# Optimization experiments

Hardware: AMD Instinct MI355X
Metric: run time of the kernel (lower is better)

## Reference

```python
import jax, jax.numpy as jnp
import numpy as np

N = 262144
C_IN = 128
C_OUT = 128
K = 9


def setup_inputs() -> dict:
    key = jax.random.key(0)
    k1, k2, k3, k4 = jax.random.split(key, 4)
    features = jax.random.normal(k1, (N, C_IN), dtype=jnp.float32)
    neigh_idx = jax.random.randint(k2, (N, K), 0, N, dtype=jnp.int64)
    # nn.Linear(9*in_channels, out_channels): weight [out, 9*in], bias [out]
    fan_in = K * C_IN
    W = jax.random.normal(k3, (C_OUT, fan_in), dtype=jnp.float32) / np.sqrt(fan_in)
    b = jax.random.normal(k4, (C_OUT,), dtype=jnp.float32) * 0.01
    return {"features": features, "neigh_idx": neigh_idx, "W": W, "b": b}


def reference(features, neigh_idx, W, b):
    n = features.shape[0]
    # pad row of zeros at index n; redirect -1 neighbors to it
    feat_padded = jnp.concatenate([features, jnp.zeros((1, features.shape[1]), features.dtype)], axis=0)
    gather_idx = jnp.where(neigh_idx == -1, n, neigh_idx)
    col = feat_padded[gather_idx]              # [N, 9, C_in]
    col_flat = col.reshape(n, -1)              # [N, 9*C_in]
    return col_flat @ W.T + b                  # [N, C_out]
```

## Files before the change

kernel.cpp:

```cpp
#include <hip/hip_runtime.h>


#define NPTS    262144
#define CIN     128
#define COUT    128
#define KNBR    9
#define KDIM    1152
#define NKS     72
#define NFRAGS  288
#define NFRAGS_PAD 296
#define MT      256

typedef __bf16  bf16x8 __attribute__((ext_vector_type(8)));
typedef float   f32x4  __attribute__((ext_vector_type(4)));
typedef float   f32x16 __attribute__((ext_vector_type(16)));

#define VMCNT(n) (((n) & 0xF) | (((n) >> 4) << 14) | (0xF << 8) | (7 << 4))

__global__ __launch_bounds__(256) void convert_feat_kernel(const float* __restrict__ f,
                                                           __bf16* __restrict__ fb) {
    size_t i = ((size_t)blockIdx.x * 256 + threadIdx.x) * 8;
    f32x4 a = __builtin_nontemporal_load((const f32x4*)(f + i));
    f32x4 b = __builtin_nontemporal_load((const f32x4*)(f + i + 4));
    bf16x8 o;
#pragma unroll
    for (int k = 0; k < 4; ++k) { o[k] = (__bf16)a[k]; o[k + 4] = (__bf16)b[k]; }
    *(bf16x8*)(fb + i) = o;
}

__global__ __launch_bounds__(256) void pack_w_kernel(const float* __restrict__ W,
                                                     __bf16* __restrict__ Wp,
                                                     __bf16* __restrict__ zrow_b) {
    if (blockIdx.x == NFRAGS / 4) {
        int t = threadIdx.x;
        if (t < CIN) zrow_b[t] = (__bf16)0.f;
        return;
    }
    int t    = blockIdx.x * 256 + threadIdx.x;
    int lane = t & 63;
    int frag = t >> 6;
    int nt = frag & 3;
    int ks = frag >> 2;
    int n  = nt * 32 + (lane & 31);
    int k0 = ks * 16 + (lane >> 5) * 8;
    const f32x4* src = (const f32x4*)(W + (size_t)n * KDIM + k0);
    f32x4 v0 = src[0], v1 = src[1];
    bf16x8 o;
#pragma unroll
    for (int i = 0; i < 4; ++i) { o[i] = (__bf16)v0[i]; o[i + 4] = (__bf16)v1[i]; }
    *(bf16x8*)(Wp + (size_t)frag * 512 + lane * 8) = o;
}

__global__ __launch_bounds__(256, 2) void qconv_kernel(
    const __bf16* __restrict__ featb,
    const int*    __restrict__ nidx,
    const __bf16* __restrict__ Wp,
    const __bf16* __restrict__ zrow,
    const float*  __restrict__ bias,
    float*        __restrict__ out)
{
    __shared__ __align__(16) char lds_raw[4 * 2 * 2 * 4096];

    const int tid  = threadIdx.x;
    const int lane = tid & 63;
    const int wave = tid >> 6;
    const int l31  = lane & 31;
    const int half = lane >> 5;
    const int rb   = blockIdx.x * MT;
    char* myLds = lds_raw + wave * 16384;

    const int srow = lane >> 3;
    const int schk = lane & 7;

    const int* ia[8];
#pragma unroll
    for (int n = 0; n < 8; ++n) {
        int rg = rb + (n >> 2) * 128 + wave * 32 + (n & 3) * 8 + srow;
        ia[n] = nidx + (size_t)rg * KNBR;
    }

    f32x16 acc[8];
#pragma unroll
    for (int a = 0; a < 8; ++a)
#pragma unroll
        for (int i = 0; i < 16; ++i) acc[a][i] = 0.f;

    const __bf16* Pst[8];
    int NPidx[8];
    bf16x8 Bb[3][4];

    auto convertP = [&](void) {
#pragma unroll
        for (int n = 0; n < 8; ++n)
            Pst[n] = (NPidx[n] >= 0) ? featb + (size_t)NPidx[n] * CIN : zrow;
    };
    auto stage_chunk = [&](int c) {
        const int buf  = c & 1;
        const int eoff = (c & 1) * 64 + (schk ^ srow) * 8;
#pragma unroll
        for (int n = 0; n < 8; ++n) {
            const int T = n >> 2, i = n & 3;
            const __bf16* g = Pst[n] + eoff;
            char* dst = myLds + buf * 8192 + T * 4096 + i * 1024;
            __builtin_amdgcn_global_load_lds(
                (const __attribute__((address_space(1))) void*)g,
                (__attribute__((address_space(3))) void*)dst,
                16, 0, 0);
        }
    };
    auto issueB = [&](int t) {
#pragma unroll
        for (int nt = 0; nt < 4; ++nt)
            Bb[t % 3][nt] = *(const bf16x8*)(Wp + (size_t)(t * 4 + nt) * 512 + lane * 8);
    };
    auto readA = [&](int buf, int T, int ksl) -> bf16x8 {
        const int s = (ksl * 2 + half) ^ (l31 & 7);
        return *(const bf16x8*)(myLds + buf * 8192 + T * 4096 + l31 * 128 + s * 16);
    };

#pragma unroll
    for (int n = 0; n < 8; ++n) NPidx[n] = ia[n][0];
    convertP();
    __builtin_amdgcn_sched_barrier(0);
    stage_chunk(0);
    __builtin_amdgcn_sched_barrier(0);
    issueB(0); issueB(1);

#pragma unroll
    for (int j = 0; j < KNBR; ++j) {
        __builtin_amdgcn_sched_barrier(0);
        if (j == 0) __builtin_amdgcn_s_waitcnt(VMCNT(8));
        else        __builtin_amdgcn_s_waitcnt(VMCNT(16));
        __builtin_amdgcn_sched_barrier(0);
        stage_chunk(2 * j + 1);
        __builtin_amdgcn_sched_barrier(0);
        {
            const int jn = (j + 1 < KNBR) ? j + 1 : KNBR - 1;
#pragma unroll
            for (int n = 0; n < 8; ++n) NPidx[n] = ia[n][jn];
#pragma unroll
            for (int ksl = 0; ksl < 4; ++ksl) {
                const int t = j * 8 + ksl;
                issueB(t + 2);
                bf16x8 a0 = readA(0, 0, ksl);
                bf16x8 a1 = readA(0, 1, ksl);
#pragma unroll
                for (int nt = 0; nt < 4; ++nt) {
                    acc[nt]     = __builtin_amdgcn_mfma_f32_32x32x16_bf16(a0, Bb[t % 3][nt], acc[nt], 0, 0, 0);
                    acc[4 + nt] = __builtin_amdgcn_mfma_f32_32x32x16_bf16(a1, Bb[t % 3][nt], acc[4 + nt], 0, 0, 0);
                }
            }
        }
        __builtin_amdgcn_sched_barrier(0);
        __builtin_amdgcn_s_waitcnt(VMCNT(24));
        __builtin_amdgcn_sched_barrier(0);
        convertP();
        stage_chunk(2 * j + 2);
        __builtin_amdgcn_sched_barrier(0);
#pragma unroll
        for (int ksl = 4; ksl < 8; ++ksl) {
            const int t = j * 8 + ksl;
            issueB(t + 2);
            bf16x8 a0 = readA(1, 0, ksl - 4);
            bf16x8 a1 = readA(1, 1, ksl - 4);
#pragma unroll
            for (int nt = 0; nt < 4; ++nt) {
                acc[nt]     = __builtin_amdgcn_mfma_f32_32x32x16_bf16(a0, Bb[t % 3][nt], acc[nt], 0, 0, 0);
                acc[4 + nt] = __builtin_amdgcn_mfma_f32_32x32x16_bf16(a1, Bb[t % 3][nt], acc[4 + nt], 0, 0, 0);
            }
        }
    }

#pragma unroll
    for (int nt = 0; nt < 4; ++nt) {
        const int col = nt * 32 + l31;
        const float bv = bias[col];
#pragma unroll
        for (int r = 0; r < 16; ++r) {
            const int row = (r & 3) + 8 * (r >> 2) + 4 * half;
            __builtin_nontemporal_store(acc[nt][r] + bv,
                &out[(size_t)(rb + wave * 32 + row) * COUT + col]);
            __builtin_nontemporal_store(acc[4 + nt][r] + bv,
                &out[(size_t)(rb + 128 + wave * 32 + row) * COUT + col]);
        }
    }
}

__global__ void qconv_naive(const float* __restrict__ feat, const int* __restrict__ nidx,
                            const float* __restrict__ W, const float* __restrict__ bias,
                            float* __restrict__ out) {
    int p = blockIdx.x, c = threadIdx.x;
    float s = bias[c];
    for (int j = 0; j < KNBR; ++j) {
        int g = nidx[(size_t)p * KNBR + j];
        if (g < 0) continue;
        const float* fr = feat + (size_t)g * CIN;
        const float* wr = W + (size_t)c * KDIM + j * CIN;
        for (int k = 0; k < CIN; ++k) s += fr[k] * wr[k];
    }
    out[(size_t)p * COUT + c] = s;
}

extern "C" void kernel_launch(void* const* d_in, const int* in_sizes, int n_in,
                              void* d_out, int out_size, void* d_ws, size_t ws_size,
                              hipStream_t stream) {
    const float* feat = (const float*)d_in[0];
    const int*   nidx = (const int*)d_in[1];
    const float* W    = (const float*)d_in[2];
    const float* bias = (const float*)d_in[3];
    float*       out  = (float*)d_out;

    const size_t FEATB_BYTES = (size_t)NPTS * CIN * 2;
    const size_t WP_BYTES    = (size_t)NFRAGS_PAD * 512 * 2;

    if (ws_size >= FEATB_BYTES + WP_BYTES + 512) {
        __bf16* featb  = (__bf16*)d_ws;
        __bf16* Wp     = (__bf16*)((char*)d_ws + FEATB_BYTES);
        __bf16* zrow_b = (__bf16*)((char*)d_ws + FEATB_BYTES + WP_BYTES);
        convert_feat_kernel<<<NPTS * CIN / (256 * 8), 256, 0, stream>>>(feat, featb);
        pack_w_kernel<<<NFRAGS / 4 + 1, 256, 0, stream>>>(W, Wp, zrow_b);
        qconv_kernel<<<NPTS / MT, 256, 0, stream>>>(featb, nidx, Wp, zrow_b, bias, out);
    } else {
        qconv_naive<<<NPTS, COUT, 0, stream>>>(feat, nidx, W, bias, out);
    }
}
```

Baseline: 358.8 us.

## Deepen gather pipeline by staging chunks earlier and use 32-bit gather offsets

Restructures the per-neighbor loop so each half-chunk's gather into LDS is issued one phase earlier, mid-way through the previous MFMA block after an LDS-read wait. This keeps two chunks in flight and hides gather latency better. Gather addresses become 32-bit byte offsets from the bf16 feature base, and the zero row is reached through a fixed offset instead of a separate pointer. The index-pointer arrays are collapsed into two base pointers. The risks are more VGPR pressure and the correctness of the hand-tuned vmcnt and lgkmcnt values, since an LDS buffer is overwritten while it may still be read.

```diff
diff --git a/kernel.cpp b/kernel.cpp
--- a/kernel.cpp
+++ b/kernel.cpp
@@ -6,16 +6,17 @@
 #define COUT    128
 #define KNBR    9
 #define KDIM    1152
-#define NKS     72
 #define NFRAGS  288
 #define NFRAGS_PAD 296
 #define MT      256
+#define ZOFFB   67411968u
 
 typedef __bf16  bf16x8 __attribute__((ext_vector_type(8)));
 typedef float   f32x4  __attribute__((ext_vector_type(4)));
 typedef float   f32x16 __attribute__((ext_vector_type(16)));
 
 #define VMCNT(n) (((n) & 0xF) | (((n) >> 4) << 14) | (0xF << 8) | (7 << 4))
+#define LGKM0    (0xF | (3 << 14) | (7 << 4))
 
 __global__ __launch_bounds__(256) void convert_feat_kernel(const float* __restrict__ f,
                                                            __bf16* __restrict__ fb) {
@@ -55,7 +56,6 @@
     const __bf16* __restrict__ featb,
     const int*    __restrict__ nidx,
     const __bf16* __restrict__ Wp,
-    const __bf16* __restrict__ zrow,
     const float*  __restrict__ bias,
     float*        __restrict__ out)
 {
@@ -71,13 +71,10 @@
 
     const int srow = lane >> 3;
     const int schk = lane & 7;
-
-    const int* ia[8];
-#pragma unroll
-    for (int n = 0; n < 8; ++n) {
-        int rg = rb + (n >> 2) * 128 + wave * 32 + (n & 3) * 8 + srow;
-        ia[n] = nidx + (size_t)rg * KNBR;
-    }
+    const int sxor = (schk ^ srow) * 16;
+
+    const int* iab0 = nidx + (size_t)(rb + wave * 32 + srow) * KNBR;
+    const int* iab1 = iab0 + 128 * KNBR;
 
     f32x16 acc[8];
 #pragma unroll
@@ -85,23 +82,26 @@
 #pragma unroll
         for (int i = 0; i < 16; ++i) acc[a][i] = 0.f;
 
-    const __bf16* Pst[8];
-    int NPidx[8];
+    int      NPidx[8];
+    unsigned NPoff[8];
     bf16x8 Bb[3][4];
 
+    auto loadIdx = [&](int jn) {
+#pragma unroll
+        for (int n = 0; n < 8; ++n)
+            NPidx[n] = ((n >> 2) ? iab1 : iab0)[(n & 3) * 8 * KNBR + jn];
+    };
     auto convertP = [&](void) {
 #pragma unroll
         for (int n = 0; n < 8; ++n)
-            Pst[n] = (NPidx[n] >= 0) ? featb + (size_t)NPidx[n] * CIN : zrow;
+            NPoff[n] = (NPidx[n] >= 0) ? ((unsigned)NPidx[n] << 8) : ZOFFB;
     };
     auto stage_chunk = [&](int c) {
-        const int buf  = c & 1;
-        const int eoff = (c & 1) * 64 + (schk ^ srow) * 8;
+        const int eoff = (c & 1) * 128 + sxor;
 #pragma unroll
         for (int n = 0; n < 8; ++n) {
-            const int T = n >> 2, i = n & 3;
-            const __bf16* g = Pst[n] + eoff;
-            char* dst = myLds + buf * 8192 + T * 4096 + i * 1024;
+            const char* g = (const char*)featb + (NPoff[n] + eoff);
+            char* dst = myLds + (c & 1) * 8192 + (n >> 2) * 4096 + (n & 3) * 1024;
             __builtin_amdgcn_global_load_lds(
                 (const __attribute__((address_space(1))) void*)g,
                 (__attribute__((address_space(3))) void*)dst,
@@ -118,44 +118,46 @@
         return *(const bf16x8*)(myLds + buf * 8192 + T * 4096 + l31 * 128 + s * 16);
     };
 
-#pragma unroll
-    for (int n = 0; n < 8; ++n) NPidx[n] = ia[n][0];
+    loadIdx(0);
     convertP();
     __builtin_amdgcn_sched_barrier(0);
     stage_chunk(0);
     __builtin_amdgcn_sched_barrier(0);
+    stage_chunk(1);
+    __builtin_amdgcn_sched_barrier(0);
+    loadIdx(1);
+    __builtin_amdgcn_sched_barrier(0);
     issueB(0); issueB(1);
 
 #pragma unroll
     for (int j = 0; j < KNBR; ++j) {
         __builtin_amdgcn_sched_barrier(0);
-        if (j == 0) __builtin_amdgcn_s_waitcnt(VMCNT(8));
+        if (j == 0) __builtin_amdgcn_s_waitcnt(VMCNT(16));
+        else        __builtin_amdgcn_s_waitcnt(VMCNT(24));
+        __builtin_amdgcn_sched_barrier(0);
+#pragma unroll
+        for (int ksl = 0; ksl < 4; ++ksl) {
+            const int t = j * 8 + ksl;
+            issueB(t + 2);
+            bf16x8 a0 = readA(0, 0, ksl);
+            bf16x8 a1 = readA(0, 1, ksl);
+            if (ksl == 3) {
+                __builtin_amdgcn_sched_barrier(0);
+                __builtin_amdgcn_s_waitcnt(LGKM0);
+                __builtin_amdgcn_sched_barrier(0);
+                convertP();
+                stage_chunk(2 * j + 2);
+                __builtin_amdgcn_sched_barrier(0);
+            }
+#pragma unroll
+            for (int nt = 0; nt < 4; ++nt) {
+                acc[nt]     = __builtin_amdgcn_mfma_f32_32x32x16_bf16(a0, Bb[t % 3][nt], acc[nt], 0, 0, 0);
+                acc[4 + nt] = __builtin_amdgcn_mfma_f32_32x32x16_bf16(a1, Bb[t % 3][nt], acc[4 + nt], 0, 0, 0);
+            }
+        }
+        __builtin_amdgcn_sched_barrier(0);
+        if (j == 0) __builtin_amdgcn_s_waitcnt(VMCNT(32));
         else        __builtin_amdgcn_s_waitcnt(VMCNT(16));
-        __builtin_amdgcn_sched_barrier(0);
-        stage_chunk(2 * j + 1);
-        __builtin_amdgcn_sched_barrier(0);
-        {
-            const int jn = (j + 1 < KNBR) ? j + 1 : KNBR - 1;
-#pragma unroll
-            for (int n = 0; n < 8; ++n) NPidx[n] = ia[n][jn];
-#pragma unroll
-            for (int ksl = 0; ksl < 4; ++ksl) {
-                const int t = j * 8 + ksl;
-                issueB(t + 2);
-                bf16x8 a0 = readA(0, 0, ksl);
-                bf16x8 a1 = readA(0, 1, ksl);
-#pragma unroll
-                for (int nt = 0; nt < 4; ++nt) {
-                    acc[nt]     = __builtin_amdgcn_mfma_f32_32x32x16_bf16(a0, Bb[t % 3][nt], acc[nt], 0, 0, 0);
-                    acc[4 + nt] = __builtin_amdgcn_mfma_f32_32x32x16_bf16(a1, Bb[t % 3][nt], acc[4 + nt], 0, 0, 0);
-                }
-            }
-        }
-        __builtin_amdgcn_sched_barrier(0);
-        __builtin_amdgcn_s_waitcnt(VMCNT(24));
-        __builtin_amdgcn_sched_barrier(0);
-        convertP();
-        stage_chunk(2 * j + 2);
         __builtin_amdgcn_sched_barrier(0);
 #pragma unroll
         for (int ksl = 4; ksl < 8; ++ksl) {
@@ -163,6 +165,14 @@
             issueB(t + 2);
             bf16x8 a0 = readA(1, 0, ksl - 4);
             bf16x8 a1 = readA(1, 1, ksl - 4);
+            if (ksl == 7) {
+                __builtin_amdgcn_sched_barrier(0);
+                __builtin_amdgcn_s_waitcnt(LGKM0);
+                __builtin_amdgcn_sched_barrier(0);
+                loadIdx((j + 2 <= KNBR - 1) ? j + 2 : KNBR - 1);
+                stage_chunk(2 * j + 3);
+                __builtin_amdgcn_sched_barrier(0);
+            }
 #pragma unroll
             for (int nt = 0; nt < 4; ++nt) {
                 acc[nt]     = __builtin_amdgcn_mfma_f32_32x32x16_bf16(a0, Bb[t % 3][nt], acc[nt], 0, 0, 0);
@@ -170,6 +180,10 @@
             }
         }
     }
+
+    __builtin_amdgcn_sched_barrier(0);
+    __builtin_amdgcn_s_waitcnt(VMCNT(0));
+    __builtin_amdgcn_sched_barrier(0);
 
 #pragma unroll
     for (int nt = 0; nt < 4; ++nt) {
@@ -219,7 +233,7 @@
         __bf16* zrow_b = (__bf16*)((char*)d_ws + FEATB_BYTES + WP_BYTES);
         convert_feat_kernel<<<NPTS * CIN / (256 * 8), 256, 0, stream>>>(feat, featb);
         pack_w_kernel<<<NFRAGS / 4 + 1, 256, 0, stream>>>(W, Wp, zrow_b);
-        qconv_kernel<<<NPTS / MT, 256, 0, stream>>>(featb, nidx, Wp, zrow_b, bias, out);
+        qconv_kernel<<<NPTS / MT, 256, 0, stream>>>(featb, nidx, Wp, bias, out);
     } else {
         qconv_naive<<<NPTS, COUT, 0, stream>>>(feat, nidx, W, bias, out);
     }
```

Result: faster. 345.2 us (-3.8%).
